# Performance work log

Hardware: AMD Instinct MI355X
Metric: run time of the kernel (lower is better)

The kernel has to match this reference:

```python
import jax, jax.numpy as jnp
import numpy as np

B, T, W, D, NT = 32, 512, 250, 768, 2  # batch, subtokens, words, sim_dim, num_tags


def setup_inputs() -> dict:
    key = jax.random.key(0)
    ks = jax.random.split(key, 20)
    s = 0.05
    # words_ids: 2 subtokens per word for W words, rest padding (-100)
    pos = jnp.arange(T)
    wid = jnp.where(pos < 2 * W, pos // 2, -100).astype(jnp.int64)
    words_ids = jnp.broadcast_to(wid, (B, T))
    inp = {
        'bert_out': jax.random.normal(ks[0], (B, T, D), jnp.float32),
        'words_ids': words_ids,
        'label_detect': jax.random.randint(ks[1], (B, W), 0, NT).astype(jnp.int64),
        'w_ih_l0': jax.random.normal(ks[2], (4 * D, D), jnp.float32) * s,
        'w_hh_l0': jax.random.normal(ks[3], (4 * D, D), jnp.float32) * s,
        'b_l0': jax.random.normal(ks[4], (4 * D,), jnp.float32) * s,
        'w_ih_l0r': jax.random.normal(ks[5], (4 * D, D), jnp.float32) * s,
        'w_hh_l0r': jax.random.normal(ks[6], (4 * D, D), jnp.float32) * s,
        'b_l0r': jax.random.normal(ks[7], (4 * D,), jnp.float32) * s,
        'w_ih_l1': jax.random.normal(ks[8], (4 * D, 2 * D), jnp.float32) * s,
        'w_hh_l1': jax.random.normal(ks[9], (4 * D, D), jnp.float32) * s,
        'b_l1': jax.random.normal(ks[10], (4 * D,), jnp.float32) * s,
        'w_ih_l1r': jax.random.normal(ks[11], (4 * D, 2 * D), jnp.float32) * s,
        'w_hh_l1r': jax.random.normal(ks[12], (4 * D, D), jnp.float32) * s,
        'b_l1r': jax.random.normal(ks[13], (4 * D,), jnp.float32) * s,
        'w_lin': jax.random.normal(ks[14], (NT, 2 * D), jnp.float32) * s,
        'b_lin': jax.random.normal(ks[15], (NT,), jnp.float32) * s,
        'crf_start': jax.random.normal(ks[16], (NT,), jnp.float32) * 0.1,
        'crf_end': jax.random.normal(ks[17], (NT,), jnp.float32) * 0.1,
        'crf_trans': jax.random.normal(ks[18], (NT, NT), jnp.float32) * 0.1,
    }
    return inp


def first_subtoken_gather(bert_out, words_ids):
    # For each word w in [0, W): embedding of its FIRST subtoken.
    # (matches torch.unique(sorted)+first-element-per-group on HF word_ids)
    pos = jnp.arange(T)
    mask = words_ids[:, None, :] == jnp.arange(W)[None, :, None]  # [B, W, T]
    first_idx = jnp.min(jnp.where(mask, pos[None, None, :], T - 1), axis=-1)  # [B, W]
    return jnp.take_along_axis(bert_out, first_idx[..., None], axis=1)  # [B, W, D]


def lstm_dir(x, w_ih, w_hh, b, reverse):
    # x: [B, S, In] -> [B, S, H]; PyTorch gate order i, f, g, o
    H = w_hh.shape[1]
    pre = jnp.einsum('bsi,gi->bsg', x, w_ih) + b  # b = b_ih + b_hh
    if reverse:
        pre = pre[:, ::-1]
    def step(carry, p_t):
        h, c = carry
        g = p_t + h @ w_hh.T
        i, f, gg, o = jnp.split(g, 4, axis=-1)
        c = jax.nn.sigmoid(f) * c + jax.nn.sigmoid(i) * jnp.tanh(gg)
        h = jax.nn.sigmoid(o) * jnp.tanh(c)
        return (h, c), h
    h0 = jnp.zeros((x.shape[0], H), x.dtype)
    _, hs = jax.lax.scan(step, (h0, h0), jnp.swapaxes(pre, 0, 1))
    hs = jnp.swapaxes(hs, 0, 1)
    if reverse:
        hs = hs[:, ::-1]
    return hs


def crf_log_likelihood(emis, tags, start, end, trans):
    # emis: [B, S, K]; tags: [B, S]; mask = all ones; reduction='mean'
    S = emis.shape[1]
    # numerator
    t0 = tags[:, 0]
    emis_score = jnp.sum(jnp.take_along_axis(emis, tags[..., None], axis=-1)[..., 0], axis=1)
    trans_score = jnp.sum(trans[tags[:, :-1], tags[:, 1:]], axis=1)
    num = start[t0] + emis_score + trans_score + end[tags[:, -1]]
    # partition (forward algorithm)
    alpha0 = start[None, :] + emis[:, 0]  # [B, K]
    def step(alpha, e_t):
        alpha = jax.nn.logsumexp(alpha[:, :, None] + trans[None] + e_t[:, None, :], axis=1)
        return alpha, None
    alpha, _ = jax.lax.scan(step, alpha0, jnp.swapaxes(emis[:, 1:], 0, 1))
    logZ = jax.nn.logsumexp(alpha + end[None, :], axis=-1)
    return jnp.mean(num - logZ)


def crf_decode(emis, start, end, trans):
    # Viterbi, mask = all ones. Returns [B, S] int32.
    score0 = start[None, :] + emis[:, 0]
    def fwd(score, e_t):
        cand = score[:, :, None] + trans[None]          # [B, K, K]
        bp = jnp.argmax(cand, axis=1)                    # [B, K]
        score = jnp.max(cand, axis=1) + e_t
        return score, bp
    score, hist = jax.lax.scan(fwd, score0, jnp.swapaxes(emis[:, 1:], 0, 1))
    last = jnp.argmax(score + end[None, :], axis=-1)     # [B]
    def back(tag, bp_t):
        prev = jnp.take_along_axis(bp_t, tag[:, None], axis=1)[:, 0]
        return prev, prev
    _, prevs = jax.lax.scan(back, last, hist, reverse=True)
    path = jnp.concatenate([jnp.swapaxes(prevs, 0, 1), last[:, None]], axis=1)
    return path.astype(jnp.int32)


def reference(bert_out, words_ids, label_detect,
              w_ih_l0, w_hh_l0, b_l0, w_ih_l0r, w_hh_l0r, b_l0r,
              w_ih_l1, w_hh_l1, b_l1, w_ih_l1r, w_hh_l1r, b_l1r,
              w_lin, b_lin, crf_start, crf_end, crf_trans):
    feat = first_subtoken_gather(bert_out, words_ids)                      # [B, W, D]
    h1 = jnp.concatenate([lstm_dir(feat, w_ih_l0, w_hh_l0, b_l0, False),
                          lstm_dir(feat, w_ih_l0r, w_hh_l0r, b_l0r, True)], axis=-1)
    h2 = jnp.concatenate([lstm_dir(h1, w_ih_l1, w_hh_l1, b_l1, False),
                          lstm_dir(h1, w_ih_l1r, w_hh_l1r, b_l1r, True)], axis=-1)
    logits = h2 @ w_lin.T + b_lin                                           # [B, W, 2]
    ner_prob = jax.nn.softmax(logits, axis=-1)
    llh = crf_log_likelihood(ner_prob, label_detect, crf_start, crf_end, crf_trans)
    path = crf_decode(ner_prob, crf_start, crf_end, crf_trans)
    loss = -1.0 * llh
    return path, ner_prob, loss
```

## Files before the change

kernel.cpp:

```cpp
#include <hip/hip_runtime.h>
#include <cmath>

#define B_ 32
#define T_ 512
#define W_ 250
#define D_ 768
#define H_ 768
#define G_ 3072
#define NT_ 2

__global__ void first_idx_kernel(const int* __restrict__ words_ids, int* __restrict__ fidx) {
  int i = blockIdx.x * blockDim.x + threadIdx.x;
  if (i >= B_ * W_) return;
  int b = i / W_, w = i % W_;
  const int* row = words_ids + (size_t)b * T_;
  int idx = T_ - 1;
  for (int t = 0; t < T_; ++t) {
    if (row[t] == w) { idx = t; break; }
  }
  fidx[i] = idx;
}

__global__ void gather_kernel(const float* __restrict__ bert_out, const int* __restrict__ fidx,
                              float* __restrict__ feat) {
  int i = blockIdx.x * blockDim.x + threadIdx.x;
  const int nv = D_ / 4;
  if (i >= B_ * W_ * nv) return;
  int bw = i / nv, d4 = i % nv;
  int b = bw / W_, w = bw % W_;
  int t = fidx[bw];
  float4 v = ((const float4*)(bert_out + ((size_t)b * T_ + t) * D_))[d4];
  ((float4*)(feat + ((size_t)w * B_ + b) * D_))[d4] = v;
}

__global__ __launch_bounds__(256) void gemm_bias_kernel(
    const float* __restrict__ A, const float* __restrict__ Bm,
    const float* __restrict__ bias, float* __restrict__ C,
    int M, int N, int K) {
  __shared__ float As[2][16][132];
  __shared__ float Bs[2][16][132];
  const int tid = threadIdx.x;
  const int row0 = blockIdx.x * 128;
  const int col0 = blockIdx.y * 128;
  const int tx = tid & 15;
  const int ty = tid >> 4;
  const int lr = tid >> 1;
  const int lk = (tid & 1) * 8;

  int ar = row0 + lr;
  if (ar >= M) ar = M - 1;
  const float* __restrict__ Ap = A + (size_t)ar * K + lk;
  const float* __restrict__ Bp = Bm + (size_t)(col0 + lr) * K + lk;

  float acc[8][8];
#pragma unroll
  for (int i = 0; i < 8; ++i)
#pragma unroll
    for (int j = 0; j < 8; ++j) acc[i][j] = 0.0f;

  const int nk = K >> 4;

  {
    float4 a0 = *(const float4*)(Ap + 0);
    float4 a1 = *(const float4*)(Ap + 4);
    float4 b0 = *(const float4*)(Bp + 0);
    float4 b1 = *(const float4*)(Bp + 4);
    As[0][lk + 0][lr] = a0.x; As[0][lk + 1][lr] = a0.y; As[0][lk + 2][lr] = a0.z; As[0][lk + 3][lr] = a0.w;
    As[0][lk + 4][lr] = a1.x; As[0][lk + 5][lr] = a1.y; As[0][lk + 6][lr] = a1.z; As[0][lk + 7][lr] = a1.w;
    Bs[0][lk + 0][lr] = b0.x; Bs[0][lk + 1][lr] = b0.y; Bs[0][lk + 2][lr] = b0.z; Bs[0][lk + 3][lr] = b0.w;
    Bs[0][lk + 4][lr] = b1.x; Bs[0][lk + 5][lr] = b1.y; Bs[0][lk + 6][lr] = b1.z; Bs[0][lk + 7][lr] = b1.w;
  }
  __syncthreads();

  for (int t = 0; t < nk; ++t) {
    const int cur = t & 1;
    float4 a0, a1, b0, b1;
    const bool pf = (t + 1 < nk);
    if (pf) {
      const int k0 = (t + 1) << 4;
      a0 = *(const float4*)(Ap + k0);
      a1 = *(const float4*)(Ap + k0 + 4);
      b0 = *(const float4*)(Bp + k0);
      b1 = *(const float4*)(Bp + k0 + 4);
    }
#pragma unroll
    for (int k = 0; k < 16; ++k) {
      float a[8], b[8];
      *(float4*)&a[0] = *(const float4*)&As[cur][k][ty * 8];
      *(float4*)&a[4] = *(const float4*)&As[cur][k][ty * 8 + 4];
      *(float4*)&b[0] = *(const float4*)&Bs[cur][k][tx * 8];
      *(float4*)&b[4] = *(const float4*)&Bs[cur][k][tx * 8 + 4];
#pragma unroll
      for (int i = 0; i < 8; ++i)
#pragma unroll
        for (int j = 0; j < 8; ++j) acc[i][j] += a[i] * b[j];
    }
    if (pf) {
      const int nxt = cur ^ 1;
      As[nxt][lk + 0][lr] = a0.x; As[nxt][lk + 1][lr] = a0.y; As[nxt][lk + 2][lr] = a0.z; As[nxt][lk + 3][lr] = a0.w;
      As[nxt][lk + 4][lr] = a1.x; As[nxt][lk + 5][lr] = a1.y; As[nxt][lk + 6][lr] = a1.z; As[nxt][lk + 7][lr] = a1.w;
      Bs[nxt][lk + 0][lr] = b0.x; Bs[nxt][lk + 1][lr] = b0.y; Bs[nxt][lk + 2][lr] = b0.z; Bs[nxt][lk + 3][lr] = b0.w;
      Bs[nxt][lk + 4][lr] = b1.x; Bs[nxt][lk + 5][lr] = b1.y; Bs[nxt][lk + 6][lr] = b1.z; Bs[nxt][lk + 7][lr] = b1.w;
    }
    __syncthreads();
  }

#pragma unroll
  for (int i = 0; i < 8; ++i) {
    int r = row0 + ty * 8 + i;
    if (r < M) {
#pragma unroll
      for (int j = 0; j < 8; ++j) {
        int c = col0 + tx * 8 + j;
        C[(size_t)r * N + c] = acc[i][j] + bias[c];
      }
    }
  }
}

__global__ __launch_bounds__(256) void lstm_step_kernel(
    const float* __restrict__ pre_f, const float* __restrict__ pre_r,
    const float* __restrict__ whh_f, const float* __restrict__ whh_r,
    float* __restrict__ out, float* __restrict__ hbuf, float* __restrict__ cbuf,
    int s0, int sl, int Cc) {
  const int wg = blockIdx.x;
  const int dir = wg >> 7;
  const int lw = wg & 127;
  const float* __restrict__ pre = dir ? pre_r : pre_f;
  const float* __restrict__ whh = dir ? whh_r : whh_f;
  float* hb = hbuf + (size_t)dir * 2 * B_ * H_;
  float* cb = cbuf + (size_t)dir * B_ * H_;
  const int tid = threadIdx.x;
  const int b = tid & 31;
  const int rg = tid >> 5;
  const int u0 = lw * 6;

  const int s = s0 + sl;
  const int w = dir ? (W_ - 1 - s) : s;
  const int prow = dir ? (Cc - 1 - sl) : sl;

  __shared__ float w_lds[24][H_];
  __shared__ float h_lds[32][260];
  __shared__ float g_lds[32][24];

  const int lr0 = rg, lr1 = rg + 8, lr2 = rg + 16;
  const int gr0 = (lr0 / 6) * H_ + u0 + (lr0 % 6);
  const int gr1 = (lr1 / 6) * H_ + u0 + (lr1 % 6);
  const int gr2 = (lr2 / 6) * H_ + u0 + (lr2 % 6);

  const float* __restrict__ pbt = pre + ((size_t)prow * B_ + b) * G_;
  float acc0 = pbt[gr0];
  float acc1 = pbt[gr1];
  float acc2 = pbt[gr2];

  if (s > 0) {
#pragma unroll
    for (int v = 0; v < 18; ++v) {
      int i = v * 256 + tid;
      int r = i / 192;
      int j = i - r * 192;
      int grow = (r / 6) * H_ + u0 + (r % 6);
      *(float4*)&w_lds[r][j * 4] = *(const float4*)(whh + (size_t)grow * H_ + j * 4);
    }
    const float* __restrict__ hprev = hb + (size_t)(s & 1) * B_ * H_;
    for (int kc = 0; kc < H_; kc += 256) {
      __syncthreads();
#pragma unroll
      for (int v = 0; v < 8; ++v) {
        int e = v * 1024 + tid * 4;
        int bb = e >> 8;
        int kk = e & 255;
        float4 hv = *(const float4*)(hprev + (size_t)bb * H_ + kc + kk);
        *(float4*)&h_lds[bb][kk] = hv;
      }
      __syncthreads();
      const float* wp0 = &w_lds[lr0][kc];
      const float* wp1 = &w_lds[lr1][kc];
      const float* wp2 = &w_lds[lr2][kc];
      const float* hl = &h_lds[b][0];
#pragma unroll 4
      for (int k = 0; k < 256; k += 4) {
        float4 hv = *(const float4*)(hl + k);
        float4 w0v = *(const float4*)(wp0 + k);
        float4 w1v = *(const float4*)(wp1 + k);
        float4 w2v = *(const float4*)(wp2 + k);
        acc0 += hv.x * w0v.x + hv.y * w0v.y + hv.z * w0v.z + hv.w * w0v.w;
        acc1 += hv.x * w1v.x + hv.y * w1v.y + hv.z * w1v.z + hv.w * w1v.w;
        acc2 += hv.x * w2v.x + hv.y * w2v.y + hv.z * w2v.z + hv.w * w2v.w;
      }
    }
  }

  g_lds[b][lr0] = acc0;
  g_lds[b][lr1] = acc1;
  g_lds[b][lr2] = acc2;
  __syncthreads();
  if (tid < 192) {
    const int ui = tid >> 5;
    const float gi = g_lds[b][ui];
    const float gf = g_lds[b][6 + ui];
    const float gg = g_lds[b][12 + ui];
    const float go = g_lds[b][18 + ui];
    const float si = 1.0f / (1.0f + expf(-gi));
    const float sf = 1.0f / (1.0f + expf(-gf));
    const float so = 1.0f / (1.0f + expf(-go));
    const float cprev = (s == 0) ? 0.0f : cb[(size_t)b * H_ + u0 + ui];
    const float c = sf * cprev + si * tanhf(gg);
    cb[(size_t)b * H_ + u0 + ui] = c;
    const float h = so * tanhf(c);
    float* __restrict__ hnext = hb + (size_t)((s + 1) & 1) * B_ * H_;
    hnext[(size_t)b * H_ + u0 + ui] = h;
    out[((size_t)w * B_ + b) * (2 * H_) + (size_t)dir * H_ + u0 + ui] = h;
  }
}

__global__ void logits_softmax_kernel(const float* __restrict__ h2, const float* __restrict__ w_lin,
                                      const float* __restrict__ b_lin, float* __restrict__ prob) {
  int i = blockIdx.x * blockDim.x + threadIdx.x;
  if (i >= B_ * W_) return;
  int b = i / W_, w = i % W_;
  const float4* x = (const float4*)(h2 + ((size_t)w * B_ + b) * (2 * H_));
  const float4* w0 = (const float4*)(w_lin);
  const float4* w1 = (const float4*)(w_lin + 2 * H_);
  float l0 = 0.f, l1 = 0.f;
#pragma unroll 4
  for (int k = 0; k < (2 * H_) / 4; ++k) {
    float4 xv = x[k];
    float4 a = w0[k];
    float4 c = w1[k];
    l0 += xv.x * a.x + xv.y * a.y + xv.z * a.z + xv.w * a.w;
    l1 += xv.x * c.x + xv.y * c.y + xv.z * c.z + xv.w * c.w;
  }
  l0 += b_lin[0];
  l1 += b_lin[1];
  float m = fmaxf(l0, l1);
  float e0 = expf(l0 - m), e1 = expf(l1 - m);
  float s = e0 + e1;
  prob[2 * (size_t)i] = e0 / s;
  prob[2 * (size_t)i + 1] = e1 / s;
}

__device__ __forceinline__ float lse2(float a, float b) {
  float m = fmaxf(a, b);
  return m + logf(expf(a - m) + expf(b - m));
}

__global__ void crf_llh_kernel(const float* __restrict__ emis, const int* __restrict__ tags,
                               const float* __restrict__ start, const float* __restrict__ endv,
                               const float* __restrict__ trans, float* __restrict__ loss_out) {
  int tid = threadIdx.x;
  float val = 0.f;
  if (tid < B_) {
    const float* e = emis + (size_t)tid * W_ * NT_;
    const int* tg = tags + (size_t)tid * W_;
    const float t00 = trans[0], t01 = trans[1], t10 = trans[2], t11 = trans[3];
    int tp = tg[0];
    float num = start[tp] + e[tp];
    float a0 = start[0] + e[0];
    float a1 = start[1] + e[1];
    for (int s = 1; s < W_; ++s) {
      int ts = tg[s];
      num += e[2 * s + ts] + trans[tp * 2 + ts];
      tp = ts;
      float n0 = lse2(a0 + t00, a1 + t10) + e[2 * s];
      float n1 = lse2(a0 + t01, a1 + t11) + e[2 * s + 1];
      a0 = n0;
      a1 = n1;
    }
    num += endv[tp];
    float logZ = lse2(a0 + endv[0], a1 + endv[1]);
    val = num - logZ;
  }
  for (int off = 32; off > 0; off >>= 1) val += __shfl_down(val, off, 64);
  if (tid == 0) loss_out[0] = -(val / (float)B_);
}

__global__ void crf_decode_kernel(const float* __restrict__ emis,
                                  const float* __restrict__ start, const float* __restrict__ endv,
                                  const float* __restrict__ trans, float* __restrict__ path_out) {
  int b = blockIdx.x * blockDim.x + threadIdx.x;
  if (b >= B_) return;
  const float* e = emis + (size_t)b * W_ * NT_;
  const float t00 = trans[0], t01 = trans[1], t10 = trans[2], t11 = trans[3];
  float s0 = start[0] + e[0];
  float s1 = start[1] + e[1];
  unsigned long long bp0[4] = {0ull, 0ull, 0ull, 0ull};
  unsigned long long bp1[4] = {0ull, 0ull, 0ull, 0ull};
  for (int s = 1; s < W_; ++s) {
    float c00 = s0 + t00, c10 = s1 + t10;
    float c01 = s0 + t01, c11 = s1 + t11;
    int b0 = (c10 > c00) ? 1 : 0;
    int b1 = (c11 > c01) ? 1 : 0;
    float m0 = b0 ? c10 : c00;
    float m1 = b1 ? c11 : c01;
    int idx = s - 1;
    bp0[idx >> 6] |= ((unsigned long long)b0) << (idx & 63);
    bp1[idx >> 6] |= ((unsigned long long)b1) << (idx & 63);
    s0 = m0 + e[2 * s];
    s1 = m1 + e[2 * s + 1];
  }
  int tag = ((s1 + endv[1]) > (s0 + endv[0])) ? 1 : 0;
  path_out[(size_t)b * W_ + (W_ - 1)] = (float)tag;
  for (int s = W_ - 2; s >= 0; --s) {
    unsigned long long word = tag ? bp1[s >> 6] : bp0[s >> 6];
    tag = (int)((word >> (s & 63)) & 1ull);
    path_out[(size_t)b * W_ + s] = (float)tag;
  }
}

extern "C" void kernel_launch(void* const* d_in, const int* in_sizes, int n_in,
                              void* d_out, int out_size, void* d_ws, size_t ws_size,
                              hipStream_t stream) {
  const float* bert_out = (const float*)d_in[0];
  const int* words_ids = (const int*)d_in[1];
  const int* label_detect = (const int*)d_in[2];
  const float* w_ih_l0 = (const float*)d_in[3];
  const float* w_hh_l0 = (const float*)d_in[4];
  const float* b_l0 = (const float*)d_in[5];
  const float* w_ih_l0r = (const float*)d_in[6];
  const float* w_hh_l0r = (const float*)d_in[7];
  const float* b_l0r = (const float*)d_in[8];
  const float* w_ih_l1 = (const float*)d_in[9];
  const float* w_hh_l1 = (const float*)d_in[10];
  const float* b_l1 = (const float*)d_in[11];
  const float* w_ih_l1r = (const float*)d_in[12];
  const float* w_hh_l1r = (const float*)d_in[13];
  const float* b_l1r = (const float*)d_in[14];
  const float* w_lin = (const float*)d_in[15];
  const float* b_lin = (const float*)d_in[16];
  const float* crf_start = (const float*)d_in[17];
  const float* crf_end = (const float*)d_in[18];
  const float* crf_trans = (const float*)d_in[19];

  float* out = (float*)d_out;
  float* path_out = out;
  float* prob_out = out + B_ * W_;
  float* loss_out = out + B_ * W_ * 3;

  auto need = [](int c) -> size_t { return 4ull * (24731456ull + 196608ull * (size_t)c); };
  int C = 10;
  if (ws_size >= need(250)) C = 250;
  else if (ws_size >= need(125)) C = 125;
  else if (ws_size >= need(50)) C = 50;
  else if (ws_size >= need(25)) C = 25;
  const int nchunk = W_ / C;
  const size_t CBG = (size_t)C * B_ * G_;

  float* h2 = (float*)d_ws;
  float* feat = h2;
  float* h1 = h2 + 12288000;
  float* preA = h1 + 12288000;
  float* preB = preA + CBG;
  float* hbuf = preB + CBG;
  float* cbuf = hbuf + 2 * 2 * B_ * H_;
  int* fidx = (int*)(cbuf + 2 * B_ * H_);

  first_idx_kernel<<<(B_ * W_ + 255) / 256, 256, 0, stream>>>(words_ids, fidx);
  gather_kernel<<<(B_ * W_ * (D_ / 4) + 255) / 256, 256, 0, stream>>>(bert_out, fidx, feat);

  const int Mc = C * B_;
  dim3 ggrid((Mc + 127) / 128, G_ / 128);

  for (int ch = 0; ch < nchunk; ++ch) {
    const int s0 = ch * C;
    gemm_bias_kernel<<<ggrid, 256, 0, stream>>>(feat + (size_t)s0 * B_ * D_, w_ih_l0, b_l0, preA, Mc, G_, D_);
    gemm_bias_kernel<<<ggrid, 256, 0, stream>>>(feat + (size_t)(W_ - C - s0) * B_ * D_, w_ih_l0r, b_l0r, preB, Mc, G_, D_);
    for (int sl = 0; sl < C; ++sl) {
      lstm_step_kernel<<<dim3(256), dim3(256), 0, stream>>>(preA, preB, w_hh_l0, w_hh_l0r, h1, hbuf, cbuf, s0, sl, C);
    }
  }

  for (int ch = 0; ch < nchunk; ++ch) {
    const int s0 = ch * C;
    gemm_bias_kernel<<<ggrid, 256, 0, stream>>>(h1 + (size_t)s0 * B_ * (2 * H_), w_ih_l1, b_l1, preA, Mc, G_, 2 * H_);
    gemm_bias_kernel<<<ggrid, 256, 0, stream>>>(h1 + (size_t)(W_ - C - s0) * B_ * (2 * H_), w_ih_l1r, b_l1r, preB, Mc, G_, 2 * H_);
    for (int sl = 0; sl < C; ++sl) {
      lstm_step_kernel<<<dim3(256), dim3(256), 0, stream>>>(preA, preB, w_hh_l1, w_hh_l1r, h2, hbuf, cbuf, s0, sl, C);
    }
  }

  logits_softmax_kernel<<<(B_ * W_ + 255) / 256, 256, 0, stream>>>(h2, w_lin, b_lin, prob_out);

  crf_llh_kernel<<<1, 64, 0, stream>>>(prob_out, label_detect, crf_start, crf_end, crf_trans, loss_out);
  crf_decode_kernel<<<1, 64, 0, stream>>>(prob_out, crf_start, crf_end, crf_trans, path_out);
}
```

Measured before the change: 13.02 ms.

## Register-tile LSTM recurrent matvec over rows and batches with padded LDS and shuffle reduction

Restructures the per-step recurrent matvec so each thread computes a 6-row by 4-batch register tile over a 32-wide k slice, instead of 3 rows for a single batch. Each LDS load now feeds more FMAs, and the lanes' partial sums are combined with cross-lane shuffles. The weight and h LDS buffers get padding every 32 floats to avoid bank conflicts. Pre-gate and previous-cell loads are hoisted to the start of the step. The cost is more registers, which may lower occupancy, plus the added shuffle reduction.

```diff
diff --git a/kernel.cpp b/kernel.cpp
--- a/kernel.cpp
+++ b/kernel.cpp
@@ -131,38 +131,54 @@
   float* hb = hbuf + (size_t)dir * 2 * B_ * H_;
   float* cb = cbuf + (size_t)dir * B_ * H_;
   const int tid = threadIdx.x;
-  const int b = tid & 31;
-  const int rg = tid >> 5;
   const int u0 = lw * 6;
 
   const int s = s0 + sl;
   const int w = dir ? (W_ - 1 - s) : s;
   const int prow = dir ? (Cc - 1 - sl) : sl;
 
-  __shared__ float w_lds[24][H_];
-  __shared__ float h_lds[32][260];
+  const int rgrp = tid >> 6;
+  const int lane = tid & 63;
+  const int kgrp = lane >> 3;
+  const int bgrp = lane & 7;
+
+  __shared__ float w_lds[24 * 860];
+  __shared__ float h_lds[32 * 284];
   __shared__ float g_lds[32][24];
 
-  const int lr0 = rg, lr1 = rg + 8, lr2 = rg + 16;
-  const int gr0 = (lr0 / 6) * H_ + u0 + (lr0 % 6);
-  const int gr1 = (lr1 / 6) * H_ + u0 + (lr1 % 6);
-  const int gr2 = (lr2 / 6) * H_ + u0 + (lr2 % 6);
-
-  const float* __restrict__ pbt = pre + ((size_t)prow * B_ + b) * G_;
-  float acc0 = pbt[gr0];
-  float acc1 = pbt[gr1];
-  float acc2 = pbt[gr2];
+  const int cui = tid >> 5;
+  const int cb_ = tid & 31;
+  float pre_g0 = 0.f, pre_g1 = 0.f, pre_g2 = 0.f, pre_g3 = 0.f, cprev = 0.f;
+  if (tid < 192) {
+    const float* pbt = pre + ((size_t)prow * B_ + cb_) * G_;
+    pre_g0 = pbt[0 * H_ + u0 + cui];
+    pre_g1 = pbt[1 * H_ + u0 + cui];
+    pre_g2 = pbt[2 * H_ + u0 + cui];
+    pre_g3 = pbt[3 * H_ + u0 + cui];
+    if (s > 0) cprev = cb[(size_t)cb_ * H_ + u0 + cui];
+  }
+
+  float acc[6][4];
+#pragma unroll
+  for (int r = 0; r < 6; ++r)
+#pragma unroll
+    for (int j = 0; j < 4; ++j) acc[r][j] = 0.0f;
 
   if (s > 0) {
 #pragma unroll
     for (int v = 0; v < 18; ++v) {
       int i = v * 256 + tid;
-      int r = i / 192;
-      int j = i - r * 192;
-      int grow = (r / 6) * H_ + u0 + (r % 6);
-      *(float4*)&w_lds[r][j * 4] = *(const float4*)(whh + (size_t)grow * H_ + j * 4);
-    }
+      int r24 = i / 192;
+      int f4 = i - r24 * 192;
+      int k = f4 * 4;
+      int grow = (r24 / 6) * H_ + u0 + (r24 % 6);
+      *(float4*)&w_lds[r24 * 860 + k + 4 * (k >> 5)] =
+          *(const float4*)(whh + (size_t)grow * H_ + k);
+    }
+
     const float* __restrict__ hprev = hb + (size_t)(s & 1) * B_ * H_;
+    const int kl0 = kgrp * 32;
+
     for (int kc = 0; kc < H_; kc += 256) {
       __syncthreads();
 #pragma unroll
@@ -170,47 +186,71 @@
         int e = v * 1024 + tid * 4;
         int bb = e >> 8;
         int kk = e & 255;
-        float4 hv = *(const float4*)(hprev + (size_t)bb * H_ + kc + kk);
-        *(float4*)&h_lds[bb][kk] = hv;
+        *(float4*)&h_lds[bb * 284 + kk + 4 * (kk >> 5)] =
+            *(const float4*)(hprev + (size_t)bb * H_ + kc + kk);
       }
       __syncthreads();
-      const float* wp0 = &w_lds[lr0][kc];
-      const float* wp1 = &w_lds[lr1][kc];
-      const float* wp2 = &w_lds[lr2][kc];
-      const float* hl = &h_lds[b][0];
+
+      const int wbase = kc + kl0;
 #pragma unroll 4
-      for (int k = 0; k < 256; k += 4) {
-        float4 hv = *(const float4*)(hl + k);
-        float4 w0v = *(const float4*)(wp0 + k);
-        float4 w1v = *(const float4*)(wp1 + k);
-        float4 w2v = *(const float4*)(wp2 + k);
-        acc0 += hv.x * w0v.x + hv.y * w0v.y + hv.z * w0v.z + hv.w * w0v.w;
-        acc1 += hv.x * w1v.x + hv.y * w1v.y + hv.z * w1v.z + hv.w * w1v.w;
-        acc2 += hv.x * w2v.x + hv.y * w2v.y + hv.z * w2v.z + hv.w * w2v.w;
+      for (int t = 0; t < 8; ++t) {
+        const int kl = kl0 + t * 4;
+        const int ka = wbase + t * 4;
+        const int hoff = kl + 4 * (kl >> 5);
+        const int woff = ka + 4 * (ka >> 5);
+        float4 h4_0 = *(const float4*)&h_lds[(4 * bgrp + 0) * 284 + hoff];
+        float4 h4_1 = *(const float4*)&h_lds[(4 * bgrp + 1) * 284 + hoff];
+        float4 h4_2 = *(const float4*)&h_lds[(4 * bgrp + 2) * 284 + hoff];
+        float4 h4_3 = *(const float4*)&h_lds[(4 * bgrp + 3) * 284 + hoff];
+#pragma unroll
+        for (int r = 0; r < 6; ++r) {
+          float4 w4 = *(const float4*)&w_lds[(rgrp * 6 + r) * 860 + woff];
+          acc[r][0] += h4_0.x * w4.x + h4_0.y * w4.y + h4_0.z * w4.z + h4_0.w * w4.w;
+          acc[r][1] += h4_1.x * w4.x + h4_1.y * w4.y + h4_1.z * w4.z + h4_1.w * w4.w;
+          acc[r][2] += h4_2.x * w4.x + h4_2.y * w4.y + h4_2.z * w4.z + h4_2.w * w4.w;
+          acc[r][3] += h4_3.x * w4.x + h4_3.y * w4.y + h4_3.z * w4.z + h4_3.w * w4.w;
+        }
       }
     }
-  }
-
-  g_lds[b][lr0] = acc0;
-  g_lds[b][lr1] = acc1;
-  g_lds[b][lr2] = acc2;
+
+#pragma unroll
+    for (int r = 0; r < 6; ++r)
+#pragma unroll
+      for (int j = 0; j < 4; ++j) {
+        float a = acc[r][j];
+        a += __shfl_xor(a, 8, 64);
+        a += __shfl_xor(a, 16, 64);
+        a += __shfl_xor(a, 32, 64);
+        acc[r][j] = a;
+      }
+    if (kgrp == 0) {
+#pragma unroll
+      for (int r = 0; r < 6; ++r)
+#pragma unroll
+        for (int j = 0; j < 4; ++j)
+          g_lds[4 * bgrp + j][rgrp * 6 + r] = acc[r][j];
+    }
+  }
+
   __syncthreads();
+
   if (tid < 192) {
-    const int ui = tid >> 5;
-    const float gi = g_lds[b][ui];
-    const float gf = g_lds[b][6 + ui];
-    const float gg = g_lds[b][12 + ui];
-    const float go = g_lds[b][18 + ui];
+    float gi = pre_g0, gf = pre_g1, gg = pre_g2, go = pre_g3;
+    if (s > 0) {
+      gi += g_lds[cb_][cui];
+      gf += g_lds[cb_][6 + cui];
+      gg += g_lds[cb_][12 + cui];
+      go += g_lds[cb_][18 + cui];
+    }
     const float si = 1.0f / (1.0f + expf(-gi));
     const float sf = 1.0f / (1.0f + expf(-gf));
     const float so = 1.0f / (1.0f + expf(-go));
-    const float cprev = (s == 0) ? 0.0f : cb[(size_t)b * H_ + u0 + ui];
     const float c = sf * cprev + si * tanhf(gg);
-    cb[(size_t)b * H_ + u0 + ui] = c;
+    cb[(size_t)cb_ * H_ + u0 + cui] = c;
     const float h = so * tanhf(c);
     float* __restrict__ hnext = hb + (size_t)((s + 1) & 1) * B_ * H_;
-    hnext[(size_t)b * H_ + u0 + ui] = h;
-    out[((size_t)w * B_ + b) * (2 * H_) + (size_t)dir * H_ + u0 + ui] = h;
+    hnext[(size_t)cb_ * H_ + u0 + cui] = h;
+    out[((size_t)w * B_ + cb_) * (2 * H_) + (size_t)dir * H_ + u0 + cui] = h;
   }
 }
 
```

Result: faster. 11.60 ms (-10.9%).
